# Optimization experiments

Measured on AMD Instinct MI355X. Metric: run time of the kernel, lower is better.

The kernel has to match this reference:

```python
import jax, jax.numpy as jnp
import numpy as np

B, N, C, H = 4, 4096, 512, 16  # batch, seq (=input_resolution), dim, num_heads


def setup_inputs() -> dict:
    key = jax.random.key(0)
    k1, k2, k3, k4 = jax.random.split(key, 4)
    x = jax.random.normal(k1, (B, N, C), jnp.float32)
    Wqk = jax.random.normal(k2, (C, 2 * C), jnp.float32) / np.sqrt(C)
    bqk = jnp.zeros((2 * C,), jnp.float32)
    lepe_w = jax.random.normal(k3, (C, 1, 3), jnp.float32) * 0.1  # depthwise conv, groups=C
    lepe_b = jnp.zeros((C,), jnp.float32)
    return {"x": x, "Wqk": Wqk, "bqk": bqk, "lepe_w": lepe_w, "lepe_b": lepe_b}


def _rope(x):
    # x: [b, n, c]; 1D RoPE over the sequence axis, k_max = c // 2 pairs.
    b, n, c = x.shape
    k_max = c // 2
    theta = 1.0 / (10000.0 ** (jnp.arange(k_max, dtype=jnp.float32) / k_max))
    ang = jnp.arange(n, dtype=jnp.float32)[:, None] * theta  # [n, k_max]
    cos, sin = jnp.cos(ang), jnp.sin(ang)
    xr, xi = x[..., 0::2], x[..., 1::2]  # consecutive (re, im) pairs
    out = jnp.stack([xr * cos - xi * sin, xr * sin + xi * cos], axis=-1)
    return out.reshape(b, n, c)


def reference(x, Wqk, bqk, lepe_w, lepe_b):
    b, n, c = x.shape
    h = H
    d = c // h
    qk = x @ Wqk + bqk  # [b, n, 2c]
    q = jax.nn.elu(qk[..., :c]) + 1.0
    k = jax.nn.elu(qk[..., c:]) + 1.0
    q_rope = _rope(q).reshape(b, n, h, d).transpose(0, 2, 1, 3)  # [b,h,n,d]
    k_rope = _rope(k).reshape(b, n, h, d).transpose(0, 2, 1, 3)
    qh = q.reshape(b, n, h, d).transpose(0, 2, 1, 3)
    kh = k.reshape(b, n, h, d).transpose(0, 2, 1, 3)
    v = x.reshape(b, n, h, d).transpose(0, 2, 1, 3)
    # normalizer z = 1 / (q . mean_n(k) + eps)
    kmean = kh.mean(axis=2)  # [b,h,d]
    z = 1.0 / (jnp.einsum('bhnd,bhd->bhn', qh, kmean) + 1e-6)  # [b,h,n]
    # kv = (k_rope^T / sqrt(n)) @ (v / sqrt(n))
    kv = jnp.einsum('bhnd,bhne->bhde', k_rope, v) / n  # [b,h,d,d]
    out = jnp.einsum('bhnd,bhde->bhne', q_rope, kv) * z[..., None]  # [b,h,n,d]
    out = out.transpose(0, 2, 1, 3).reshape(b, n, c)
    # LePE: depthwise conv1d over sequence on v (v reassembled == x)
    vt = x.transpose(0, 2, 1)  # [b, c, n]
    lepe = jax.lax.conv_general_dilated(
        vt, lepe_w, window_strides=(1,), padding=((1, 1),),
        feature_group_count=c, dimension_numbers=('NCH', 'OIH', 'NCH'))
    lepe = lepe + lepe_b[None, :, None]
    return out + lepe.transpose(0, 2, 1)
```

## Files before the change

### kernel.cpp

```cpp
#include <hip/hip_runtime.h>

typedef unsigned short u16;
typedef u16   u16x8 __attribute__((ext_vector_type(8)));
typedef short s16x8 __attribute__((ext_vector_type(8)));
typedef float f32x4 __attribute__((ext_vector_type(4)));

__device__ __forceinline__ float b2f(u16 u) {
    return __uint_as_float(((unsigned)u) << 16);
}
__device__ __forceinline__ u16 f2b(float f) {
    unsigned x = __float_as_uint(f);
    x += 0x7fffu + ((x >> 16) & 1u);
    return (u16)(x >> 16);
}
__device__ __forceinline__ void gload_lds(const u16* g, u16* l) {
    __builtin_amdgcn_global_load_lds(
        (const __attribute__((address_space(1))) unsigned int*)g,
        (__attribute__((address_space(3))) unsigned int*)l, 16, 0, 0);
}

#define THETA_SCALE 0.05190512648261f

__global__ __launch_bounds__(256)
void k_prep(const float* __restrict__ X, u16* __restrict__ Xb,
            const float* __restrict__ W, u16* __restrict__ WT,
            float* __restrict__ kvz) {
    if (blockIdx.x < 4096) {
        size_t i = (size_t)(blockIdx.x * 256 + threadIdx.x) * 8;
        float4 a = *(const float4*)(X + i);
        float4 b = *(const float4*)(X + i + 4);
        u16x8 r;
        r[0] = f2b(a.x); r[1] = f2b(a.y); r[2] = f2b(a.z); r[3] = f2b(a.w);
        r[4] = f2b(b.x); r[5] = f2b(b.y); r[6] = f2b(b.z); r[7] = f2b(b.w);
        *(u16x8*)(Xb + i) = r;
    } else if (blockIdx.x < 4608) {
        __shared__ float tile[32][33];
        int bid = blockIdx.x - 4096;
        int c0 = (bid & 31) * 32;
        int r0 = (bid >> 5) * 32;
        int tx = threadIdx.x & 31;
        int ty = threadIdx.x >> 5;
        #pragma unroll
        for (int i = 0; i < 4; ++i) {
            int r = ty + i * 8;
            tile[r][tx] = W[(size_t)(r0 + r) * 1024 + c0 + tx];
        }
        __syncthreads();
        #pragma unroll
        for (int i = 0; i < 4; ++i) {
            int r = ty + i * 8;
            WT[(size_t)(c0 + r) * 512 + r0 + tx] = f2b(tile[tx][r]);
        }
    } else {
        size_t i = (size_t)(blockIdx.x - 4608) * 1024 + threadIdx.x * 4;
        *(float4*)(kvz + i) = make_float4(0.f, 0.f, 0.f, 0.f);
    }
}

__global__ __launch_bounds__(512, 2)
void k_gemm(const u16* __restrict__ Xb, const u16* __restrict__ WT,
            const float* __restrict__ bqk,
            u16* __restrict__ Qb, u16* __restrict__ Kb) {
    __shared__ u16 As[2][256 * 64];
    __shared__ u16 Bs[2][256 * 64];
    const int t = threadIdx.x;
    const int lin = blockIdx.x + (blockIdx.y << 6);
    const int by = (lin >> 3) & 3;
    const int bx = (lin & 7) | ((lin >> 5) << 3);
    const int m0 = bx * 256;
    const int n0 = by * 256;
    const int lane = t & 63;
    const int wave = t >> 6;
    const int wm = (wave >> 2) * 128;
    const int wn = (wave & 3) * 64;
    const int quad = lane >> 4;
    const int l16 = lane & 15;
    const int srow = lane >> 3;
    const int skc  = lane & 7;

    f32x4 acc[8][4];
    #pragma unroll
    for (int i = 0; i < 8; ++i)
        #pragma unroll
        for (int j = 0; j < 4; ++j) acc[i][j] = (f32x4){0.f, 0.f, 0.f, 0.f};

    #pragma unroll
    for (int c = 0; c < 4; ++c) {
        int row = c * 64 + wave * 8 + srow;
        int kcs = (skc ^ (row & 7)) * 8;
        gload_lds(Xb + (size_t)(m0 + row) * 512 + kcs,
                  &As[0][(c * 64 + wave * 8) * 64]);
        gload_lds(WT + (size_t)(n0 + row) * 512 + kcs,
                  &Bs[0][(c * 64 + wave * 8) * 64]);
    }

    for (int kt = 0; kt < 8; ++kt) {
        const int cur = kt & 1;
        if (kt < 7) {
            const int k0 = (kt + 1) * 64;
            #pragma unroll
            for (int c = 0; c < 4; ++c) {
                int row = c * 64 + wave * 8 + srow;
                int kcs = (skc ^ (row & 7)) * 8;
                gload_lds(Xb + (size_t)(m0 + row) * 512 + k0 + kcs,
                          &As[cur ^ 1][(c * 64 + wave * 8) * 64]);
                gload_lds(WT + (size_t)(n0 + row) * 512 + k0 + kcs,
                          &Bs[cur ^ 1][(c * 64 + wave * 8) * 64]);
            }
            asm volatile("s_waitcnt vmcnt(8)" ::: "memory");
        } else {
            asm volatile("s_waitcnt vmcnt(0)" ::: "memory");
        }
        __builtin_amdgcn_s_barrier();
        asm volatile("" ::: "memory");

        #pragma unroll
        for (int s = 0; s < 2; ++s) {
            const int cb = s * 4 + quad;
            s16x8 af[8], bf[4];
            #pragma unroll
            for (int f = 0; f < 8; ++f) {
                int row = wm + f * 16 + l16;
                af[f] = *(const s16x8*)&As[cur][row * 64 + ((cb ^ (row & 7)) * 8)];
            }
            #pragma unroll
            for (int j = 0; j < 4; ++j) {
                int row = wn + j * 16 + l16;
                bf[j] = *(const s16x8*)&Bs[cur][row * 64 + ((cb ^ (row & 7)) * 8)];
            }
            __builtin_amdgcn_s_setprio(1);
            #pragma unroll
            for (int f = 0; f < 8; ++f)
                #pragma unroll
                for (int j = 0; j < 4; ++j)
                    acc[f][j] = __builtin_amdgcn_mfma_f32_16x16x32_bf16(
                        af[f], bf[j], acc[f][j], 0, 0, 0);
            __builtin_amdgcn_s_setprio(0);
        }
        asm volatile("" ::: "memory");
        __builtin_amdgcn_s_barrier();
    }

    u16* O = (n0 < 512) ? Qb : Kb;
    #pragma unroll
    for (int f = 0; f < 8; ++f)
        #pragma unroll
        for (int j = 0; j < 4; ++j) {
            int col = n0 + wn + j * 16 + l16;
            float bias = bqk[col];
            int gc = col & 511;
            #pragma unroll
            for (int r = 0; r < 4; ++r) {
                int grow = m0 + wm + f * 16 + quad * 4 + r;
                float v = acc[f][j][r] + bias;
                v = v > 0.f ? v + 1.f : __expf(v);
                O[(size_t)grow * 512 + gc] = f2b(v);
            }
        }
}

__global__ __launch_bounds__(256)
void k_kv(const u16* __restrict__ Kb, const u16* __restrict__ Xb,
          float* __restrict__ kvbuf, float* __restrict__ ksum) {
    const int bh = blockIdx.x;
    const int b = bh >> 4, h = bh & 15;
    const int nb = blockIdx.y * 512;
    __shared__ u16 krT[32 * 72];
    __shared__ u16 vT[32 * 72];
    __shared__ float red[64 * 36];
    const int t = threadIdx.x;
    const int row = t >> 2;
    const int c8 = (t & 3) * 8;
    const int rot_w = 16 * ((c8 >> 3) & 3);
    const int lane = t & 63;
    const int wave = t >> 6;
    const int quad = lane >> 4;
    const int l16 = lane & 15;
    const int dq = (wave >> 1) * 16;
    const int eq = (wave & 1) * 16;
    const int ca = dq + l16;
    const int cb2 = eq + l16;
    const int rot_a = 16 * ((ca >> 3) & 3);
    const int rot_b = 16 * ((cb2 >> 3) & 3);

    float ksl[8] = {0, 0, 0, 0, 0, 0, 0, 0};
    f32x4 acc = {0.f, 0.f, 0.f, 0.f};

    float th[4];
    #pragma unroll
    for (int p = 0; p < 4; ++p)
        th[p] = exp2f(-THETA_SCALE * (float)(h * 16 + (c8 >> 1) + p));

    size_t base0 = (size_t)(b * 4096 + nb + row) * 512 + h * 32 + c8;
    u16x8 k8 = *(const u16x8*)(Kb + base0);
    u16x8 v8 = *(const u16x8*)(Xb + base0);

    for (int pass = 0; pass < 8; ++pass) {
        int n = nb + pass * 64 + row;
        u16x8 k8n, v8n;
        if (pass < 7) {
            size_t basen = (size_t)(b * 4096 + n + 64) * 512 + h * 32 + c8;
            k8n = *(const u16x8*)(Kb + basen);
            v8n = *(const u16x8*)(Xb + basen);
        }
        float kf[8], kr[8];
        #pragma unroll
        for (int j = 0; j < 8; ++j) kf[j] = b2f(k8[j]);
        #pragma unroll
        for (int p = 0; p < 4; ++p) {
            float sv, cv;
            sincosf((float)n * th[p], &sv, &cv);
            kr[2 * p]     = kf[2 * p] * cv - kf[2 * p + 1] * sv;
            kr[2 * p + 1] = kf[2 * p] * sv + kf[2 * p + 1] * cv;
        }
        #pragma unroll
        for (int j = 0; j < 8; ++j) ksl[j] += kf[j];
        if (pass) __syncthreads();
        int colw = (row + rot_w) & 63;
        #pragma unroll
        for (int j = 0; j < 8; ++j) {
            krT[(c8 + j) * 72 + colw] = f2b(kr[j]);
            vT[(c8 + j) * 72 + colw] = v8[j];
        }
        __syncthreads();
        #pragma unroll
        for (int ks = 0; ks < 64; ks += 32) {
            s16x8 a4 = *(const s16x8*)&krT[ca * 72 + ((ks + quad * 8 + rot_a) & 63)];
            s16x8 b4 = *(const s16x8*)&vT[cb2 * 72 + ((ks + quad * 8 + rot_b) & 63)];
            acc = __builtin_amdgcn_mfma_f32_16x16x32_bf16(a4, b4, acc, 0, 0, 0);
        }
        k8 = k8n; v8 = v8n;
    }

    #pragma unroll
    for (int r = 0; r < 4; ++r)
        atomicAdd(&kvbuf[(size_t)bh * 1024 + (dq + quad * 4 + r) * 32 + eq + l16],
                  acc[r]);

    __syncthreads();
    *(float4*)&red[row * 36 + c8]     = make_float4(ksl[0], ksl[1], ksl[2], ksl[3]);
    *(float4*)&red[row * 36 + c8 + 4] = make_float4(ksl[4], ksl[5], ksl[6], ksl[7]);
    __syncthreads();
    if (t < 32) {
        float s = 0.f;
        for (int r = 0; r < 64; ++r) s += red[r * 36 + t];
        atomicAdd(&ksum[bh * 32 + t], s);
    }
}

__global__ __launch_bounds__(256)
void k_out(const u16* __restrict__ Qb, const u16* __restrict__ Xb,
           const float* __restrict__ kvbuf, const float* __restrict__ ksum,
           const float* __restrict__ lw, const float* __restrict__ lb,
           float* __restrict__ OUT) {
    const int b = blockIdx.x >> 6;
    const int nb = (blockIdx.x & 63) * 64;
    const int hbase = blockIdx.y * 4;
    __shared__ u16 kvT_s[32 * 36];
    __shared__ u16 qr_s[64 * 36];
    __shared__ float out_s[64 * 36];
    __shared__ float ks_s[32];
    __shared__ float z_s[64];
    const int t = threadIdx.x;
    const int row = t >> 2;
    const int c4 = t & 3;
    const int e0 = c4 * 8;
    const int lane = t & 63;
    const int wave = t >> 6;
    const int quad = lane >> 4;
    const int l16 = lane & 15;
    const float invN = 1.f / 4096.f;
    const int n = nb + row;
    const size_t rowbase = (size_t)(b * 4096 + n) * 512;

    float4 kvv = *(const float4*)&kvbuf[(size_t)(b * 16 + hbase) * 1024 + t * 4];
    float ksv = (t < 32) ? ksum[(b * 16 + hbase) * 32 + t] : 0.f;
    u16x8 q8 = *(const u16x8*)(Qb + rowbase + hbase * 32 + e0);

    for (int hh = 0; hh < 4; ++hh) {
        const int h = hbase + hh;
        const int bh = b * 16 + h;
        if (hh) __syncthreads();
        {
            int id = t * 4;
            int d = id >> 5, e = id & 31;
            kvT_s[(e + 0) * 36 + d] = f2b(kvv.x * invN);
            kvT_s[(e + 1) * 36 + d] = f2b(kvv.y * invN);
            kvT_s[(e + 2) * 36 + d] = f2b(kvv.z * invN);
            kvT_s[(e + 3) * 36 + d] = f2b(kvv.w * invN);
        }
        if (t < 32) ks_s[t] = ksv * invN;
        __syncthreads();

        float qf[8];
        #pragma unroll
        for (int j = 0; j < 8; ++j) qf[j] = b2f(q8[j]);
        float part = 0.f;
        #pragma unroll
        for (int j = 0; j < 8; ++j) part += qf[j] * ks_s[e0 + j];
        u16x8 qr8;
        #pragma unroll
        for (int p = 0; p < 4; ++p) {
            float th = exp2f(-THETA_SCALE * (float)(h * 16 + c4 * 4 + p));
            float sv, cv;
            sincosf((float)n * th, &sv, &cv);
            qr8[2 * p]     = f2b(qf[2 * p] * cv - qf[2 * p + 1] * sv);
            qr8[2 * p + 1] = f2b(qf[2 * p] * sv + qf[2 * p + 1] * cv);
        }
        *(u16x8*)&qr_s[row * 36 + e0] = qr8;
        part += __shfl_xor(part, 1);
        part += __shfl_xor(part, 2);
        if (c4 == 0) z_s[row] = 1.f / (part + 1e-6f);

        const int cb = h * 32 + e0;
        u16x8 xc = *(const u16x8*)(Xb + rowbase + cb);
        u16x8 xm = {0, 0, 0, 0, 0, 0, 0, 0};
        u16x8 xp = {0, 0, 0, 0, 0, 0, 0, 0};
        if (n > 0)    xm = *(const u16x8*)(Xb + rowbase - 512 + cb);
        if (n < 4095) xp = *(const u16x8*)(Xb + rowbase + 512 + cb);
        float wv[24];
        #pragma unroll
        for (int q = 0; q < 6; ++q)
            *(float4*)&wv[q * 4] = *(const float4*)(lw + cb * 3 + q * 4);
        float lbv[8];
        *(float4*)&lbv[0] = *(const float4*)(lb + cb);
        *(float4*)&lbv[4] = *(const float4*)(lb + cb + 4);
        if (hh < 3) {
            kvv = *(const float4*)&kvbuf[(size_t)(bh + 1) * 1024 + t * 4];
            if (t < 32) ksv = ksum[(bh + 1) * 32 + t];
            q8 = *(const u16x8*)(Qb + rowbase + (h + 1) * 32 + e0);
        }
        __syncthreads();

        {
            f32x4 zero4 = {0.f, 0.f, 0.f, 0.f};
            s16x8 a4 = *(const s16x8*)&qr_s[(wave * 16 + l16) * 36 + quad * 8];
            #pragma unroll
            for (int et = 0; et < 2; ++et) {
                s16x8 b4 = *(const s16x8*)&kvT_s[(et * 16 + l16) * 36 + quad * 8];
                f32x4 cacc = __builtin_amdgcn_mfma_f32_16x16x32_bf16(
                    a4, b4, zero4, 0, 0, 0);
                #pragma unroll
                for (int r = 0; r < 4; ++r)
                    out_s[(wave * 16 + quad * 4 + r) * 36 + et * 16 + l16] = cacc[r];
            }
        }
        __syncthreads();

        const float z = z_s[row];
        float4 o0 = *(const float4*)&out_s[row * 36 + e0];
        float4 o1 = *(const float4*)&out_s[row * 36 + e0 + 4];
        float o[8] = {o0.x, o0.y, o0.z, o0.w, o1.x, o1.y, o1.z, o1.w};
        float rv[8];
        #pragma unroll
        for (int j = 0; j < 8; ++j) {
            float lep = b2f(xm[j]) * wv[3 * j] +
                        b2f(xc[j]) * wv[3 * j + 1] +
                        b2f(xp[j]) * wv[3 * j + 2] + lbv[j];
            rv[j] = o[j] * z + lep;
        }
        float* Of = OUT + rowbase + cb;
        *(float4*)Of       = make_float4(rv[0], rv[1], rv[2], rv[3]);
        *(float4*)(Of + 4) = make_float4(rv[4], rv[5], rv[6], rv[7]);
    }
}

extern "C" void kernel_launch(void* const* d_in, const int* in_sizes, int n_in,
                              void* d_out, int out_size, void* d_ws, size_t ws_size,
                              hipStream_t stream) {
    const float* x   = (const float*)d_in[0];
    const float* Wqk = (const float*)d_in[1];
    const float* bqk = (const float*)d_in[2];
    const float* lw  = (const float*)d_in[3];
    const float* lb  = (const float*)d_in[4];
    float* out = (float*)d_out;

    char* w = (char*)d_ws;
    u16* Kb      = (u16*)w;   w += (size_t)16384 * 512 * 2;
    u16* Qb      = (u16*)w;   w += (size_t)16384 * 512 * 2;
    u16* Xb      = (u16*)w;   w += (size_t)16384 * 512 * 2;
    u16* WT      = (u16*)w;   w += (size_t)1024 * 512 * 2;
    float* kvbuf = (float*)w; w += (size_t)64 * 1024 * 4;
    float* ksum  = (float*)w;

    k_prep<<<4674, 256, 0, stream>>>(x, Xb, Wqk, WT, kvbuf);
    k_gemm<<<dim3(64, 4), 512, 0, stream>>>(Xb, WT, bqk, Qb, Kb);
    k_kv<<<dim3(64, 8), 256, 0, stream>>>(Kb, Xb, kvbuf, ksum);
    k_out<<<dim3(256, 4), 256, 0, stream>>>(Qb, Xb, kvbuf, ksum, lw, lb, out);
}
```

Baseline: 139.9 us.

## Fuse four kernels into one cooperative persistent kernel with grid syncs

Replaces the four separate launches (prep, GEMM, kv reduction, output) with a single cooperative kernel of 256 blocks of 512 threads. The stages are separated by grid-wide syncs and share one 128KB LDS buffer. Each block runs two 256-thread sub-groups for the kv and output stages. The goal is to remove inter-kernel launch gaps and tail effects, at the cost of grid-sync overhead and fixed occupancy for the lighter stages.

Measured after the change: 246.6 us. 1.76x slower.

```diff
diff --git a/kernel.cpp b/kernel.cpp
--- a/kernel.cpp
+++ b/kernel.cpp
@@ -1,4 +1,6 @@
 #include <hip/hip_runtime.h>
+#include <hip/hip_cooperative_groups.h>
+namespace cg = cooperative_groups;
 
 typedef unsigned short u16;
 typedef u16   u16x8 __attribute__((ext_vector_type(8)));
@@ -21,347 +23,361 @@
 
 #define THETA_SCALE 0.05190512648261f
 
-__global__ __launch_bounds__(256)
-void k_prep(const float* __restrict__ X, u16* __restrict__ Xb,
-            const float* __restrict__ W, u16* __restrict__ WT,
-            float* __restrict__ kvz) {
-    if (blockIdx.x < 4096) {
-        size_t i = (size_t)(blockIdx.x * 256 + threadIdx.x) * 8;
-        float4 a = *(const float4*)(X + i);
-        float4 b = *(const float4*)(X + i + 4);
-        u16x8 r;
-        r[0] = f2b(a.x); r[1] = f2b(a.y); r[2] = f2b(a.z); r[3] = f2b(a.w);
-        r[4] = f2b(b.x); r[5] = f2b(b.y); r[6] = f2b(b.z); r[7] = f2b(b.w);
-        *(u16x8*)(Xb + i) = r;
-    } else if (blockIdx.x < 4608) {
-        __shared__ float tile[32][33];
-        int bid = blockIdx.x - 4096;
+__global__ __launch_bounds__(512, 2)
+void k_mega(const float* __restrict__ X, const float* __restrict__ W,
+            const float* __restrict__ bqk, const float* __restrict__ lw,
+            const float* __restrict__ lb,
+            u16* __restrict__ Xb, u16* __restrict__ WT,
+            u16* __restrict__ Qb, u16* __restrict__ Kb,
+            float* __restrict__ kvbuf, float* __restrict__ ksum,
+            float* __restrict__ OUT) {
+    __shared__ u16 SM[65536];
+    cg::grid_group gg = cg::this_grid();
+    const int t = threadIdx.x;
+    const int bId = blockIdx.x;
+
+    {
+        #pragma unroll
+        for (int it = 0; it < 8; ++it) {
+            size_t idx = (size_t)(it * 256 + bId) * 512 + t;
+            size_t i = idx * 8;
+            float4 a = *(const float4*)(X + i);
+            float4 b = *(const float4*)(X + i + 4);
+            u16x8 r;
+            r[0] = f2b(a.x); r[1] = f2b(a.y); r[2] = f2b(a.z); r[3] = f2b(a.w);
+            r[4] = f2b(b.x); r[5] = f2b(b.y); r[6] = f2b(b.z); r[7] = f2b(b.w);
+            *(u16x8*)(Xb + i) = r;
+        }
+        int idx0 = bId * 512 + t;
+        if (idx0 < 16896)
+            *(float4*)(kvbuf + idx0 * 4) = make_float4(0.f, 0.f, 0.f, 0.f);
+        int g = t >> 8, tt = t & 255;
+        float* tile = (float*)(SM + g * 2304);
+        int bid = bId * 2 + g;
         int c0 = (bid & 31) * 32;
         int r0 = (bid >> 5) * 32;
-        int tx = threadIdx.x & 31;
-        int ty = threadIdx.x >> 5;
+        int tx = tt & 31, ty = tt >> 5;
         #pragma unroll
         for (int i = 0; i < 4; ++i) {
             int r = ty + i * 8;
-            tile[r][tx] = W[(size_t)(r0 + r) * 1024 + c0 + tx];
+            tile[r * 33 + tx] = W[(size_t)(r0 + r) * 1024 + c0 + tx];
         }
         __syncthreads();
         #pragma unroll
         for (int i = 0; i < 4; ++i) {
             int r = ty + i * 8;
-            WT[(size_t)(c0 + r) * 512 + r0 + tx] = f2b(tile[tx][r]);
-        }
-    } else {
-        size_t i = (size_t)(blockIdx.x - 4608) * 1024 + threadIdx.x * 4;
-        *(float4*)(kvz + i) = make_float4(0.f, 0.f, 0.f, 0.f);
+            WT[(size_t)(c0 + r) * 512 + r0 + tx] = f2b(tile[tx * 33 + r]);
+        }
     }
-}
-
-__global__ __launch_bounds__(512, 2)
-void k_gemm(const u16* __restrict__ Xb, const u16* __restrict__ WT,
-            const float* __restrict__ bqk,
-            u16* __restrict__ Qb, u16* __restrict__ Kb) {
-    __shared__ u16 As[2][256 * 64];
-    __shared__ u16 Bs[2][256 * 64];
-    const int t = threadIdx.x;
-    const int lin = blockIdx.x + (blockIdx.y << 6);
-    const int by = (lin >> 3) & 3;
-    const int bx = (lin & 7) | ((lin >> 5) << 3);
-    const int m0 = bx * 256;
-    const int n0 = by * 256;
-    const int lane = t & 63;
-    const int wave = t >> 6;
-    const int wm = (wave >> 2) * 128;
-    const int wn = (wave & 3) * 64;
-    const int quad = lane >> 4;
-    const int l16 = lane & 15;
-    const int srow = lane >> 3;
-    const int skc  = lane & 7;
-
-    f32x4 acc[8][4];
-    #pragma unroll
-    for (int i = 0; i < 8; ++i)
-        #pragma unroll
-        for (int j = 0; j < 4; ++j) acc[i][j] = (f32x4){0.f, 0.f, 0.f, 0.f};
-
-    #pragma unroll
-    for (int c = 0; c < 4; ++c) {
-        int row = c * 64 + wave * 8 + srow;
-        int kcs = (skc ^ (row & 7)) * 8;
-        gload_lds(Xb + (size_t)(m0 + row) * 512 + kcs,
-                  &As[0][(c * 64 + wave * 8) * 64]);
-        gload_lds(WT + (size_t)(n0 + row) * 512 + kcs,
-                  &Bs[0][(c * 64 + wave * 8) * 64]);
+    gg.sync();
+
+    {
+        const int lin = bId;
+        const int by = (lin >> 3) & 3;
+        const int bx = (lin & 7) | ((lin >> 5) << 3);
+        const int m0 = bx * 256;
+        const int n0 = by * 256;
+        const int lane = t & 63;
+        const int wave = t >> 6;
+        const int wm = (wave >> 2) * 128;
+        const int wn = (wave & 3) * 64;
+        const int quad = lane >> 4;
+        const int l16 = lane & 15;
+        const int srow = lane >> 3;
+        const int skc  = lane & 7;
+        u16* As0 = SM;
+        u16* Bs0 = SM + 32768;
+
+        f32x4 acc[8][4];
+        #pragma unroll
+        for (int i = 0; i < 8; ++i)
+            #pragma unroll
+            for (int j = 0; j < 4; ++j) acc[i][j] = (f32x4){0.f, 0.f, 0.f, 0.f};
+
+        #pragma unroll
+        for (int c = 0; c < 4; ++c) {
+            int row = c * 64 + wave * 8 + srow;
+            int kcs = (skc ^ (row & 7)) * 8;
+            gload_lds(Xb + (size_t)(m0 + row) * 512 + kcs,
+                      As0 + (c * 64 + wave * 8) * 64);
+            gload_lds(WT + (size_t)(n0 + row) * 512 + kcs,
+                      Bs0 + (c * 64 + wave * 8) * 64);
+        }
+
+        for (int kt = 0; kt < 8; ++kt) {
+            const int cur = kt & 1;
+            if (kt < 7) {
+                const int k0 = (kt + 1) * 64;
+                #pragma unroll
+                for (int c = 0; c < 4; ++c) {
+                    int row = c * 64 + wave * 8 + srow;
+                    int kcs = (skc ^ (row & 7)) * 8;
+                    gload_lds(Xb + (size_t)(m0 + row) * 512 + k0 + kcs,
+                              As0 + (cur ^ 1) * 16384 + (c * 64 + wave * 8) * 64);
+                    gload_lds(WT + (size_t)(n0 + row) * 512 + k0 + kcs,
+                              Bs0 + (cur ^ 1) * 16384 + (c * 64 + wave * 8) * 64);
+                }
+                asm volatile("s_waitcnt vmcnt(8)" ::: "memory");
+            } else {
+                asm volatile("s_waitcnt vmcnt(0)" ::: "memory");
+            }
+            __builtin_amdgcn_s_barrier();
+            asm volatile("" ::: "memory");
+
+            #pragma unroll
+            for (int s = 0; s < 2; ++s) {
+                const int cb = s * 4 + quad;
+                s16x8 af[8], bf[4];
+                #pragma unroll
+                for (int f = 0; f < 8; ++f) {
+                    int row = wm + f * 16 + l16;
+                    af[f] = *(const s16x8*)&As0[cur * 16384 + row * 64 +
+                                                ((cb ^ (row & 7)) * 8)];
+                }
+                #pragma unroll
+                for (int j = 0; j < 4; ++j) {
+                    int row = wn + j * 16 + l16;
+                    bf[j] = *(const s16x8*)&Bs0[cur * 16384 + row * 64 +
+                                                ((cb ^ (row & 7)) * 8)];
+                }
+                __builtin_amdgcn_s_setprio(1);
+                #pragma unroll
+                for (int f = 0; f < 8; ++f)
+                    #pragma unroll
+                    for (int j = 0; j < 4; ++j)
+                        acc[f][j] = __builtin_amdgcn_mfma_f32_16x16x32_bf16(
+                            af[f], bf[j], acc[f][j], 0, 0, 0);
+                __builtin_amdgcn_s_setprio(0);
+            }
+            asm volatile("" ::: "memory");
+            __builtin_amdgcn_s_barrier();
+        }
+
+        u16* O = (n0 < 512) ? Qb : Kb;
+        #pragma unroll
+        for (int f = 0; f < 8; ++f)
+            #pragma unroll
+            for (int j = 0; j < 4; ++j) {
+                int col = n0 + wn + j * 16 + l16;
+                float bias = bqk[col];
+                int gc = col & 511;
+                #pragma unroll
+                for (int r = 0; r < 4; ++r) {
+                    int grow = m0 + wm + f * 16 + quad * 4 + r;
+                    float v = acc[f][j][r] + bias;
+                    v = v > 0.f ? v + 1.f : __expf(v);
+                    O[(size_t)grow * 512 + gc] = f2b(v);
+                }
+            }
     }
-
-    for (int kt = 0; kt < 8; ++kt) {
-        const int cur = kt & 1;
-        if (kt < 7) {
-            const int k0 = (kt + 1) * 64;
-            #pragma unroll
-            for (int c = 0; c < 4; ++c) {
-                int row = c * 64 + wave * 8 + srow;
-                int kcs = (skc ^ (row & 7)) * 8;
-                gload_lds(Xb + (size_t)(m0 + row) * 512 + k0 + kcs,
-                          &As[cur ^ 1][(c * 64 + wave * 8) * 64]);
-                gload_lds(WT + (size_t)(n0 + row) * 512 + k0 + kcs,
-                          &Bs[cur ^ 1][(c * 64 + wave * 8) * 64]);
-            }
-            asm volatile("s_waitcnt vmcnt(8)" ::: "memory");
-        } else {
-            asm volatile("s_waitcnt vmcnt(0)" ::: "memory");
-        }
-        __builtin_amdgcn_s_barrier();
-        asm volatile("" ::: "memory");
-
-        #pragma unroll
-        for (int s = 0; s < 2; ++s) {
-            const int cb = s * 4 + quad;
-            s16x8 af[8], bf[4];
-            #pragma unroll
-            for (int f = 0; f < 8; ++f) {
-                int row = wm + f * 16 + l16;
-                af[f] = *(const s16x8*)&As[cur][row * 64 + ((cb ^ (row & 7)) * 8)];
-            }
-            #pragma unroll
-            for (int j = 0; j < 4; ++j) {
-                int row = wn + j * 16 + l16;
-                bf[j] = *(const s16x8*)&Bs[cur][row * 64 + ((cb ^ (row & 7)) * 8)];
-            }
-            __builtin_amdgcn_s_setprio(1);
-            #pragma unroll
-            for (int f = 0; f < 8; ++f)
-                #pragma unroll
-                for (int j = 0; j < 4; ++j)
-                    acc[f][j] = __builtin_amdgcn_mfma_f32_16x16x32_bf16(
-                        af[f], bf[j], acc[f][j], 0, 0, 0);
-            __builtin_amdgcn_s_setprio(0);
-        }
-        asm volatile("" ::: "memory");
-        __builtin_amdgcn_s_barrier();
+    gg.sync();
+
+    {
+        const int g = t >> 8, tt = t & 255;
+        char* gb = (char*)SM + g * 20480;
+        u16* krT = (u16*)gb;
+        u16* vT  = (u16*)(gb + 4608);
+        float* red = (float*)(gb + 9216);
+        const int v = bId * 2 + g;
+        const int bh = v & 63;
+        const int b = bh >> 4, h = bh & 15;
+        const int nb = (v >> 6) * 512;
+        const int row = tt >> 2;
+        const int c8 = (tt & 3) * 8;
+        const int rot_w = 16 * ((c8 >> 3) & 3);
+        const int lane = tt & 63;
+        const int wave = tt >> 6;
+        const int quad = lane >> 4;
+        const int l16 = lane & 15;
+        const int dq = (wave >> 1) * 16;
+        const int eq = (wave & 1) * 16;
+        const int ca = dq + l16;
+        const int cb2 = eq + l16;
+        const int rot_a = 16 * ((ca >> 3) & 3);
+        const int rot_b = 16 * ((cb2 >> 3) & 3);
+
+        float ksl[8] = {0, 0, 0, 0, 0, 0, 0, 0};
+        f32x4 acc = {0.f, 0.f, 0.f, 0.f};
+        float th[4];
+        #pragma unroll
+        for (int p = 0; p < 4; ++p)
+            th[p] = exp2f(-THETA_SCALE * (float)(h * 16 + (c8 >> 1) + p));
+
+        size_t base0 = (size_t)(b * 4096 + nb + row) * 512 + h * 32 + c8;
+        u16x8 k8 = *(const u16x8*)(Kb + base0);
+        u16x8 v8 = *(const u16x8*)(Xb + base0);
+
+        for (int pass = 0; pass < 8; ++pass) {
+            int n = nb + pass * 64 + row;
+            u16x8 k8n, v8n;
+            if (pass < 7) {
+                size_t basen = (size_t)(b * 4096 + n + 64) * 512 + h * 32 + c8;
+                k8n = *(const u16x8*)(Kb + basen);
+                v8n = *(const u16x8*)(Xb + basen);
+            }
+            float kf[8], kr[8];
+            #pragma unroll
+            for (int j = 0; j < 8; ++j) kf[j] = b2f(k8[j]);
+            #pragma unroll
+            for (int p = 0; p < 4; ++p) {
+                float sv, cv;
+                sincosf((float)n * th[p], &sv, &cv);
+                kr[2 * p]     = kf[2 * p] * cv - kf[2 * p + 1] * sv;
+                kr[2 * p + 1] = kf[2 * p] * sv + kf[2 * p + 1] * cv;
+            }
+            #pragma unroll
+            for (int j = 0; j < 8; ++j) ksl[j] += kf[j];
+            if (pass) __syncthreads();
+            int colw = (row + rot_w) & 63;
+            #pragma unroll
+            for (int j = 0; j < 8; ++j) {
+                krT[(c8 + j) * 72 + colw] = f2b(kr[j]);
+                vT[(c8 + j) * 72 + colw] = v8[j];
+            }
+            __syncthreads();
+            #pragma unroll
+            for (int ks = 0; ks < 64; ks += 32) {
+                s16x8 a4 = *(const s16x8*)&krT[ca * 72 + ((ks + quad * 8 + rot_a) & 63)];
+                s16x8 b4 = *(const s16x8*)&vT[cb2 * 72 + ((ks + quad * 8 + rot_b) & 63)];
+                acc = __builtin_amdgcn_mfma_f32_16x16x32_bf16(a4, b4, acc, 0, 0, 0);
+            }
+            k8 = k8n; v8 = v8n;
+        }
+
+        #pragma unroll
+        for (int r = 0; r < 4; ++r)
+            atomicAdd(&kvbuf[(size_t)bh * 1024 + (dq + quad * 4 + r) * 32 + eq + l16],
+                      acc[r]);
+
+        __syncthreads();
+        *(float4*)&red[row * 36 + c8]     = make_float4(ksl[0], ksl[1], ksl[2], ksl[3]);
+        *(float4*)&red[row * 36 + c8 + 4] = make_float4(ksl[4], ksl[5], ksl[6], ksl[7]);
+        __syncthreads();
+        if (tt < 32) {
+            float s = 0.f;
+            for (int r = 0; r < 64; ++r) s += red[r * 36 + tt];
+            atomicAdd(&ksum[bh * 32 + tt], s);
+        }
     }
-
-    u16* O = (n0 < 512) ? Qb : Kb;
-    #pragma unroll
-    for (int f = 0; f < 8; ++f)
-        #pragma unroll
-        for (int j = 0; j < 4; ++j) {
-            int col = n0 + wn + j * 16 + l16;
-            float bias = bqk[col];
-            int gc = col & 511;
-            #pragma unroll
-            for (int r = 0; r < 4; ++r) {
-                int grow = m0 + wm + f * 16 + quad * 4 + r;
-                float v = acc[f][j][r] + bias;
-                v = v > 0.f ? v + 1.f : __expf(v);
-                O[(size_t)grow * 512 + gc] = f2b(v);
-            }
-        }
-}
-
-__global__ __launch_bounds__(256)
-void k_kv(const u16* __restrict__ Kb, const u16* __restrict__ Xb,
-          float* __restrict__ kvbuf, float* __restrict__ ksum) {
-    const int bh = blockIdx.x;
-    const int b = bh >> 4, h = bh & 15;
-    const int nb = blockIdx.y * 512;
-    __shared__ u16 krT[32 * 72];
-    __shared__ u16 vT[32 * 72];
-    __shared__ float red[64 * 36];
-    const int t = threadIdx.x;
-    const int row = t >> 2;
-    const int c8 = (t & 3) * 8;
-    const int rot_w = 16 * ((c8 >> 3) & 3);
-    const int lane = t & 63;
-    const int wave = t >> 6;
-    const int quad = lane >> 4;
-    const int l16 = lane & 15;
-    const int dq = (wave >> 1) * 16;
-    const int eq = (wave & 1) * 16;
-    const int ca = dq + l16;
-    const int cb2 = eq + l16;
-    const int rot_a = 16 * ((ca >> 3) & 3);
-    const int rot_b = 16 * ((cb2 >> 3) & 3);
-
-    float ksl[8] = {0, 0, 0, 0, 0, 0, 0, 0};
-    f32x4 acc = {0.f, 0.f, 0.f, 0.f};
-
-    float th[4];
-    #pragma unroll
-    for (int p = 0; p < 4; ++p)
-        th[p] = exp2f(-THETA_SCALE * (float)(h * 16 + (c8 >> 1) + p));
-
-    size_t base0 = (size_t)(b * 4096 + nb + row) * 512 + h * 32 + c8;
-    u16x8 k8 = *(const u16x8*)(Kb + base0);
-    u16x8 v8 = *(const u16x8*)(Xb + base0);
-
-    for (int pass = 0; pass < 8; ++pass) {
-        int n = nb + pass * 64 + row;
-        u16x8 k8n, v8n;
-        if (pass < 7) {
-            size_t basen = (size_t)(b * 4096 + n + 64) * 512 + h * 32 + c8;
-            k8n = *(const u16x8*)(Kb + basen);
-            v8n = *(const u16x8*)(Xb + basen);
-        }
-        float kf[8], kr[8];
-        #pragma unroll
-        for (int j = 0; j < 8; ++j) kf[j] = b2f(k8[j]);
-        #pragma unroll
-        for (int p = 0; p < 4; ++p) {
-            float sv, cv;
-            sincosf((float)n * th[p], &sv, &cv);
-            kr[2 * p]     = kf[2 * p] * cv - kf[2 * p + 1] * sv;
-            kr[2 * p + 1] = kf[2 * p] * sv + kf[2 * p + 1] * cv;
-        }
-        #pragma unroll
-        for (int j = 0; j < 8; ++j) ksl[j] += kf[j];
-        if (pass) __syncthreads();
-        int colw = (row + rot_w) & 63;
-        #pragma unroll
-        for (int j = 0; j < 8; ++j) {
-            krT[(c8 + j) * 72 + colw] = f2b(kr[j]);
-            vT[(c8 + j) * 72 + colw] = v8[j];
-        }
-        __syncthreads();
-        #pragma unroll
-        for (int ks = 0; ks < 64; ks += 32) {
-            s16x8 a4 = *(const s16x8*)&krT[ca * 72 + ((ks + quad * 8 + rot_a) & 63)];
-            s16x8 b4 = *(const s16x8*)&vT[cb2 * 72 + ((ks + quad * 8 + rot_b) & 63)];
-            acc = __builtin_amdgcn_mfma_f32_16x16x32_bf16(a4, b4, acc, 0, 0, 0);
-        }
-        k8 = k8n; v8 = v8n;
-    }
-
-    #pragma unroll
-    for (int r = 0; r < 4; ++r)
-        atomicAdd(&kvbuf[(size_t)bh * 1024 + (dq + quad * 4 + r) * 32 + eq + l16],
-                  acc[r]);
-
-    __syncthreads();
-    *(float4*)&red[row * 36 + c8]     = make_float4(ksl[0], ksl[1], ksl[2], ksl[3]);
-    *(float4*)&red[row * 36 + c8 + 4] = make_float4(ksl[4], ksl[5], ksl[6], ksl[7]);
-    __syncthreads();
-    if (t < 32) {
-        float s = 0.f;
-        for (int r = 0; r < 64; ++r) s += red[r * 36 + t];
-        atomicAdd(&ksum[bh * 32 + t], s);
-    }
-}
-
-__global__ __launch_bounds__(256)
-void k_out(const u16* __restrict__ Qb, const u16* __restrict__ Xb,
-           const float* __restrict__ kvbuf, const float* __restrict__ ksum,
-           const float* __restrict__ lw, const float* __restrict__ lb,
-           float* __restrict__ OUT) {
-    const int b = blockIdx.x >> 6;
-    const int nb = (blockIdx.x & 63) * 64;
-    const int hbase = blockIdx.y * 4;
-    __shared__ u16 kvT_s[32 * 36];
-    __shared__ u16 qr_s[64 * 36];
-    __shared__ float out_s[64 * 36];
-    __shared__ float ks_s[32];
-    __shared__ float z_s[64];
-    const int t = threadIdx.x;
-    const int row = t >> 2;
-    const int c4 = t & 3;
-    const int e0 = c4 * 8;
-    const int lane = t & 63;
-    const int wave = t >> 6;
-    const int quad = lane >> 4;
-    const int l16 = lane & 15;
-    const float invN = 1.f / 4096.f;
-    const int n = nb + row;
-    const size_t rowbase = (size_t)(b * 4096 + n) * 512;
-
-    float4 kvv = *(const float4*)&kvbuf[(size_t)(b * 16 + hbase) * 1024 + t * 4];
-    float ksv = (t < 32) ? ksum[(b * 16 + hbase) * 32 + t] : 0.f;
-    u16x8 q8 = *(const u16x8*)(Qb + rowbase + hbase * 32 + e0);
-
-    for (int hh = 0; hh < 4; ++hh) {
-        const int h = hbase + hh;
-        const int bh = b * 16 + h;
-        if (hh) __syncthreads();
-        {
-            int id = t * 4;
-            int d = id >> 5, e = id & 31;
-            kvT_s[(e + 0) * 36 + d] = f2b(kvv.x * invN);
-            kvT_s[(e + 1) * 36 + d] = f2b(kvv.y * invN);
-            kvT_s[(e + 2) * 36 + d] = f2b(kvv.z * invN);
-            kvT_s[(e + 3) * 36 + d] = f2b(kvv.w * invN);
-        }
-        if (t < 32) ks_s[t] = ksv * invN;
-        __syncthreads();
-
-        float qf[8];
-        #pragma unroll
-        for (int j = 0; j < 8; ++j) qf[j] = b2f(q8[j]);
-        float part = 0.f;
-        #pragma unroll
-        for (int j = 0; j < 8; ++j) part += qf[j] * ks_s[e0 + j];
-        u16x8 qr8;
-        #pragma unroll
-        for (int p = 0; p < 4; ++p) {
-            float th = exp2f(-THETA_SCALE * (float)(h * 16 + c4 * 4 + p));
-            float sv, cv;
-            sincosf((float)n * th, &sv, &cv);
-            qr8[2 * p]     = f2b(qf[2 * p] * cv - qf[2 * p + 1] * sv);
-            qr8[2 * p + 1] = f2b(qf[2 * p] * sv + qf[2 * p + 1] * cv);
-        }
-        *(u16x8*)&qr_s[row * 36 + e0] = qr8;
-        part += __shfl_xor(part, 1);
-        part += __shfl_xor(part, 2);
-        if (c4 == 0) z_s[row] = 1.f / (part + 1e-6f);
-
-        const int cb = h * 32 + e0;
-        u16x8 xc = *(const u16x8*)(Xb + rowbase + cb);
-        u16x8 xm = {0, 0, 0, 0, 0, 0, 0, 0};
-        u16x8 xp = {0, 0, 0, 0, 0, 0, 0, 0};
-        if (n > 0)    xm = *(const u16x8*)(Xb + rowbase - 512 + cb);
-        if (n < 4095) xp = *(const u16x8*)(Xb + rowbase + 512 + cb);
-        float wv[24];
-        #pragma unroll
-        for (int q = 0; q < 6; ++q)
-            *(float4*)&wv[q * 4] = *(const float4*)(lw + cb * 3 + q * 4);
-        float lbv[8];
-        *(float4*)&lbv[0] = *(const float4*)(lb + cb);
-        *(float4*)&lbv[4] = *(const float4*)(lb + cb + 4);
-        if (hh < 3) {
-            kvv = *(const float4*)&kvbuf[(size_t)(bh + 1) * 1024 + t * 4];
-            if (t < 32) ksv = ksum[(bh + 1) * 32 + t];
-            q8 = *(const u16x8*)(Qb + rowbase + (h + 1) * 32 + e0);
-        }
-        __syncthreads();
-
-        {
-            f32x4 zero4 = {0.f, 0.f, 0.f, 0.f};
-            s16x8 a4 = *(const s16x8*)&qr_s[(wave * 16 + l16) * 36 + quad * 8];
-            #pragma unroll
-            for (int et = 0; et < 2; ++et) {
-                s16x8 b4 = *(const s16x8*)&kvT_s[(et * 16 + l16) * 36 + quad * 8];
-                f32x4 cacc = __builtin_amdgcn_mfma_f32_16x16x32_bf16(
-                    a4, b4, zero4, 0, 0, 0);
-                #pragma unroll
-                for (int r = 0; r < 4; ++r)
-                    out_s[(wave * 16 + quad * 4 + r) * 36 + et * 16 + l16] = cacc[r];
-            }
-        }
-        __syncthreads();
-
-        const float z = z_s[row];
-        float4 o0 = *(const float4*)&out_s[row * 36 + e0];
-        float4 o1 = *(const float4*)&out_s[row * 36 + e0 + 4];
-        float o[8] = {o0.x, o0.y, o0.z, o0.w, o1.x, o1.y, o1.z, o1.w};
-        float rv[8];
-        #pragma unroll
-        for (int j = 0; j < 8; ++j) {
-            float lep = b2f(xm[j]) * wv[3 * j] +
-                        b2f(xc[j]) * wv[3 * j + 1] +
-                        b2f(xp[j]) * wv[3 * j + 2] + lbv[j];
-            rv[j] = o[j] * z + lep;
-        }
-        float* Of = OUT + rowbase + cb;
-        *(float4*)Of       = make_float4(rv[0], rv[1], rv[2], rv[3]);
-        *(float4*)(Of + 4) = make_float4(rv[4], rv[5], rv[6], rv[7]);
+    gg.sync();
+
+    {
+        const int g = t >> 8, tt = t & 255;
+        char* gb = (char*)SM + g * 20480;
+        u16* kvT_s = (u16*)gb;
+        u16* qr_s  = (u16*)(gb + 2304);
+        float* out_s = (float*)(gb + 6912);
+        float* ks_s  = (float*)(gb + 16128);
+        float* z_s   = (float*)(gb + 16256);
+        const int row = tt >> 2;
+        const int c4 = tt & 3;
+        const int e0 = c4 * 8;
+        const int lane = tt & 63;
+        const int wave = tt >> 6;
+        const int quad = lane >> 4;
+        const int l16 = lane & 15;
+        const float invN = 1.f / 4096.f;
+
+        for (int rep = 0; rep < 2; ++rep) {
+            if (rep) __syncthreads();
+            const int v = rep * 512 + bId * 2 + g;
+            const int b = (v & 255) >> 6;
+            const int nb = ((v & 255) & 63) * 64;
+            const int hbase = (v >> 8) * 4;
+            const int n = nb + row;
+            const size_t rowbase = (size_t)(b * 4096 + n) * 512;
+
+            float4 kvv = *(const float4*)&kvbuf[(size_t)(b * 16 + hbase) * 1024 + tt * 4];
+            float ksv = (tt < 32) ? ksum[(b * 16 + hbase) * 32 + tt] : 0.f;
+            u16x8 q8 = *(const u16x8*)(Qb + rowbase + hbase * 32 + e0);
+
+            for (int hh = 0; hh < 4; ++hh) {
+                const int h = hbase + hh;
+                const int bh = b * 16 + h;
+                if (hh) __syncthreads();
+                {
+                    int id = tt * 4;
+                    int d = id >> 5, e = id & 31;
+                    kvT_s[(e + 0) * 36 + d] = f2b(kvv.x * invN);
+                    kvT_s[(e + 1) * 36 + d] = f2b(kvv.y * invN);
+                    kvT_s[(e + 2) * 36 + d] = f2b(kvv.z * invN);
+                    kvT_s[(e + 3) * 36 + d] = f2b(kvv.w * invN);
+                }
+                if (tt < 32) ks_s[tt] = ksv * invN;
+                __syncthreads();
+
+                float qf[8];
+                #pragma unroll
+                for (int j = 0; j < 8; ++j) qf[j] = b2f(q8[j]);
+                float part = 0.f;
+                #pragma unroll
+                for (int j = 0; j < 8; ++j) part += qf[j] * ks_s[e0 + j];
+                u16x8 qr8;
+                #pragma unroll
+                for (int p = 0; p < 4; ++p) {
+                    float th = exp2f(-THETA_SCALE * (float)(h * 16 + c4 * 4 + p));
+                    float sv, cv;
+                    sincosf((float)n * th, &sv, &cv);
+                    qr8[2 * p]     = f2b(qf[2 * p] * cv - qf[2 * p + 1] * sv);
+                    qr8[2 * p + 1] = f2b(qf[2 * p] * sv + qf[2 * p + 1] * cv);
+                }
+                *(u16x8*)&qr_s[row * 36 + e0] = qr8;
+                part += __shfl_xor(part, 1);
+                part += __shfl_xor(part, 2);
+                if (c4 == 0) z_s[row] = 1.f / (part + 1e-6f);
+
+                const int cb = h * 32 + e0;
+                u16x8 xc = *(const u16x8*)(Xb + rowbase + cb);
+                u16x8 xm = {0, 0, 0, 0, 0, 0, 0, 0};
+                u16x8 xp = {0, 0, 0, 0, 0, 0, 0, 0};
+                if (n > 0)    xm = *(const u16x8*)(Xb + rowbase - 512 + cb);
+                if (n < 4095) xp = *(const u16x8*)(Xb + rowbase + 512 + cb);
+                float wv[24];
+                #pragma unroll
+                for (int q = 0; q < 6; ++q)
+                    *(float4*)&wv[q * 4] = *(const float4*)(lw + cb * 3 + q * 4);
+                float lbv[8];
+                *(float4*)&lbv[0] = *(const float4*)(lb + cb);
+                *(float4*)&lbv[4] = *(const float4*)(lb + cb + 4);
+                if (hh < 3) {
+                    kvv = *(const float4*)&kvbuf[(size_t)(bh + 1) * 1024 + tt * 4];
+                    if (tt < 32) ksv = ksum[(bh + 1) * 32 + tt];
+                    q8 = *(const u16x8*)(Qb + rowbase + (h + 1) * 32 + e0);
+                }
+                __syncthreads();
+
+                {
+                    f32x4 zero4 = {0.f, 0.f, 0.f, 0.f};
+                    s16x8 a4 = *(const s16x8*)&qr_s[(wave * 16 + l16) * 36 + quad * 8];
+                    #pragma unroll
+                    for (int et = 0; et < 2; ++et) {
+                        s16x8 b4 = *(const s16x8*)&kvT_s[(et * 16 + l16) * 36 + quad * 8];
+                        f32x4 cacc = __builtin_amdgcn_mfma_f32_16x16x32_bf16(
+                            a4, b4, zero4, 0, 0, 0);
+                        #pragma unroll
+                        for (int r = 0; r < 4; ++r)
+                            out_s[(wave * 16 + quad * 4 + r) * 36 + et * 16 + l16] = cacc[r];
+                    }
+                }
+                __syncthreads();
+
+                const float z = z_s[row];
+                float4 o0 = *(const float4*)&out_s[row * 36 + e0];
+                float4 o1 = *(const float4*)&out_s[row * 36 + e0 + 4];
+                float o[8] = {o0.x, o0.y, o0.z, o0.w, o1.x, o1.y, o1.z, o1.w};
+                float rv[8];
+                #pragma unroll
+                for (int j = 0; j < 8; ++j) {
+                    float lep = b2f(xm[j]) * wv[3 * j] +
+                                b2f(xc[j]) * wv[3 * j + 1] +
+                                b2f(xp[j]) * wv[3 * j + 2] + lbv[j];
+                    rv[j] = o[j] * z + lep;
+                }
+                float* Of = OUT + rowbase + cb;
+                *(float4*)Of       = make_float4(rv[0], rv[1], rv[2], rv[3]);
+                *(float4*)(Of + 4) = make_float4(rv[4], rv[5], rv[6], rv[7]);
+            }
+        }
     }
 }
 
@@ -383,8 +399,9 @@
     float* kvbuf = (float*)w; w += (size_t)64 * 1024 * 4;
     float* ksum  = (float*)w;
 
-    k_prep<<<4674, 256, 0, stream>>>(x, Xb, Wqk, WT, kvbuf);
-    k_gemm<<<dim3(64, 4), 512, 0, stream>>>(Xb, WT, bqk, Qb, Kb);
-    k_kv<<<dim3(64, 8), 256, 0, stream>>>(Kb, Xb, kvbuf, ksum);
-    k_out<<<dim3(256, 4), 256, 0, stream>>>(Qb, Xb, kvbuf, ksum, lw, lb, out);
+    void* args[] = {(void*)&x, (void*)&Wqk, (void*)&bqk, (void*)&lw, (void*)&lb,
+                    (void*)&Xb, (void*)&WT, (void*)&Qb, (void*)&Kb,
+                    (void*)&kvbuf, (void*)&ksum, (void*)&out};
+    hipLaunchCooperativeKernel((void*)k_mega, dim3(256), dim3(512),
+                               args, 0, stream);
 }
```

## Split QK GEMM k-tile into four sub-phases with interleaved quarter-tile prefetch

Applied to the files above, without the earlier changes.

Restructures the QK projection GEMM main loop into four quadrant phases (A-half × B-half). Each phase loads its fragments from LDS, issues a quarter of the global-to-LDS prefetch, and runs MFMAs, so loads are spread across the iteration rather than issued in one burst. Prefetch now runs up to two k-tiles ahead, reusing the current buffer halves once they have been consumed. It adds more barriers and hand-tuned vmcnt/lgkmcnt waits, which risks stalls or races if the counts are wrong.

After: 140.0 us. About the same (+0.0%).

```diff
diff --git a/kernel.cpp b/kernel.cpp
--- a/kernel.cpp
+++ b/kernel.cpp
@@ -20,6 +20,12 @@
 }
 
 #define THETA_SCALE 0.05190512648261f
+
+#define LGKM0 do { asm volatile("s_waitcnt lgkmcnt(0)" ::: "memory"); \
+                   __builtin_amdgcn_sched_barrier(0); } while (0)
+#define BARRIER do { asm volatile("" ::: "memory"); \
+                     __builtin_amdgcn_s_barrier(); \
+                     asm volatile("" ::: "memory"); } while (0)
 
 __global__ __launch_bounds__(256)
 void k_prep(const float* __restrict__ X, u16* __restrict__ Xb,
@@ -84,61 +90,106 @@
         #pragma unroll
         for (int j = 0; j < 4; ++j) acc[i][j] = (f32x4){0.f, 0.f, 0.f, 0.f};
 
-    #pragma unroll
-    for (int c = 0; c < 4; ++c) {
-        int row = c * 64 + wave * 8 + srow;
-        int kcs = (skc ^ (row & 7)) * 8;
-        gload_lds(Xb + (size_t)(m0 + row) * 512 + kcs,
-                  &As[0][(c * 64 + wave * 8) * 64]);
-        gload_lds(WT + (size_t)(n0 + row) * 512 + kcs,
-                  &Bs[0][(c * 64 + wave * 8) * 64]);
-    }
+    auto stageA = [&](int bufb, int half, int kt2) {
+        int k0 = kt2 * 64;
+        #pragma unroll
+        for (int l = 0; l < 2; ++l) {
+            int c = half + l * 2;
+            int r0 = c * 64 + wave * 8;
+            int row = r0 + srow;
+            int kcs = (skc ^ (row & 7)) * 8;
+            gload_lds(Xb + (size_t)(m0 + row) * 512 + k0 + kcs, &As[bufb][r0 * 64]);
+        }
+    };
+    auto stageB = [&](int bufb, int jh, int kt2) {
+        int k0 = kt2 * 64;
+        #pragma unroll
+        for (int l = 0; l < 2; ++l) {
+            int c = wave & 3;
+            int wg = jh * 4 + (wave >> 2) + l * 2;
+            int r0 = c * 64 + wg * 8;
+            int row = r0 + srow;
+            int kcs = (skc ^ (row & 7)) * 8;
+            gload_lds(WT + (size_t)(n0 + row) * 512 + k0 + kcs, &Bs[bufb][r0 * 64]);
+        }
+    };
+    auto loadA = [&](int bufb, int fh, s16x8 (&af)[4][2]) {
+        #pragma unroll
+        for (int fi = 0; fi < 4; ++fi) {
+            int row = wm + (fh * 4 + fi) * 16 + l16;
+            #pragma unroll
+            for (int ks = 0; ks < 2; ++ks) {
+                int cb = ks * 4 + quad;
+                af[fi][ks] = *(const s16x8*)&As[bufb][row * 64 + ((cb ^ (row & 7)) * 8)];
+            }
+        }
+    };
+    auto loadB = [&](int bufb, int jh, s16x8 (&bf)[2][2]) {
+        #pragma unroll
+        for (int jj = 0; jj < 2; ++jj) {
+            int row = wn + (jh * 2 + jj) * 16 + l16;
+            #pragma unroll
+            for (int ks = 0; ks < 2; ++ks) {
+                int cb = ks * 4 + quad;
+                bf[jj][ks] = *(const s16x8*)&Bs[bufb][row * 64 + ((cb ^ (row & 7)) * 8)];
+            }
+        }
+    };
+    auto mma = [&](int fh, int jh, s16x8 (&af)[4][2], s16x8 (&bf)[2][2]) {
+        __builtin_amdgcn_s_setprio(1);
+        #pragma unroll
+        for (int fi = 0; fi < 4; ++fi)
+            #pragma unroll
+            for (int jj = 0; jj < 2; ++jj) {
+                int f = fh * 4 + fi, j = jh * 2 + jj;
+                acc[f][j] = __builtin_amdgcn_mfma_f32_16x16x32_bf16(
+                    af[fi][0], bf[jj][0], acc[f][j], 0, 0, 0);
+                acc[f][j] = __builtin_amdgcn_mfma_f32_16x16x32_bf16(
+                    af[fi][1], bf[jj][1], acc[f][j], 0, 0, 0);
+            }
+        __builtin_amdgcn_s_setprio(0);
+    };
+
+    stageA(0, 0, 0);
+    stageB(0, 0, 0);
+    stageA(0, 1, 0);
+    stageB(0, 1, 0);
+    stageA(1, 0, 1);
+    stageB(1, 0, 1);
+    asm volatile("s_waitcnt vmcnt(8)" ::: "memory");
+    BARRIER;
 
     for (int kt = 0; kt < 8; ++kt) {
         const int cur = kt & 1;
+        s16x8 af[4][2], bf[2][2];
+        loadA(cur, 0, af);
+        loadB(cur, 0, bf);
+        if (kt < 7) stageA(cur ^ 1, 1, kt + 1);
+        LGKM0;
+        mma(0, 0, af, bf);
+        if (kt == 7) { asm volatile("s_waitcnt vmcnt(0)" ::: "memory"); }
+        else         { asm volatile("s_waitcnt vmcnt(6)" ::: "memory"); }
+        BARRIER;
+        loadB(cur, 1, bf);
+        if (kt < 7) stageB(cur ^ 1, 1, kt + 1);
+        LGKM0;
+        mma(0, 1, af, bf);
+        BARRIER;
+        loadA(cur, 1, af);
+        loadB(cur, 0, bf);
+        if (kt < 6) stageA(cur, 0, kt + 2);
+        LGKM0;
+        mma(1, 0, af, bf);
+        BARRIER;
+        loadB(cur, 1, bf);
+        if (kt < 6) stageB(cur, 0, kt + 2);
+        LGKM0;
+        mma(1, 1, af, bf);
         if (kt < 7) {
-            const int k0 = (kt + 1) * 64;
-            #pragma unroll
-            for (int c = 0; c < 4; ++c) {
-                int row = c * 64 + wave * 8 + srow;
-                int kcs = (skc ^ (row & 7)) * 8;
-                gload_lds(Xb + (size_t)(m0 + row) * 512 + k0 + kcs,
-                          &As[cur ^ 1][(c * 64 + wave * 8) * 64]);
-                gload_lds(WT + (size_t)(n0 + row) * 512 + k0 + kcs,
-                          &Bs[cur ^ 1][(c * 64 + wave * 8) * 64]);
-            }
-            asm volatile("s_waitcnt vmcnt(8)" ::: "memory");
-        } else {
-            asm volatile("s_waitcnt vmcnt(0)" ::: "memory");
-        }
-        __builtin_amdgcn_s_barrier();
-        asm volatile("" ::: "memory");
-
-        #pragma unroll
-        for (int s = 0; s < 2; ++s) {
-            const int cb = s * 4 + quad;
-            s16x8 af[8], bf[4];
-            #pragma unroll
-            for (int f = 0; f < 8; ++f) {
-                int row = wm + f * 16 + l16;
-                af[f] = *(const s16x8*)&As[cur][row * 64 + ((cb ^ (row & 7)) * 8)];
-            }
-            #pragma unroll
-            for (int j = 0; j < 4; ++j) {
-                int row = wn + j * 16 + l16;
-                bf[j] = *(const s16x8*)&Bs[cur][row * 64 + ((cb ^ (row & 7)) * 8)];
-            }
-            __builtin_amdgcn_s_setprio(1);
-            #pragma unroll
-            for (int f = 0; f < 8; ++f)
-                #pragma unroll
-                for (int j = 0; j < 4; ++j)
-                    acc[f][j] = __builtin_amdgcn_mfma_f32_16x16x32_bf16(
-                        af[f], bf[j], acc[f][j], 0, 0, 0);
-            __builtin_amdgcn_s_setprio(0);
-        }
-        asm volatile("" ::: "memory");
-        __builtin_amdgcn_s_barrier();
+            if (kt == 6) { asm volatile("s_waitcnt vmcnt(4)" ::: "memory"); }
+            else         { asm volatile("s_waitcnt vmcnt(8)" ::: "memory"); }
+            BARRIER;
+        }
     }
 
     u16* O = (n0 < 512) ? Qb : Kb;
```
